# Optimization experiments

Measured on AMD Instinct MI355X. Metric: run time of the kernel, lower is better.

The kernel has to match this reference:

```python
import jax, jax.numpy as jnp
import numpy as np

HAND_PARAM_DIM = 32
MASK_THRESHOLD = 0.5
MAX_SAMPLES = 1024
INF_DIST = 1.0e6
EPS = 1e-8

B, S, HW, V = 4, 16, 65536, 778


def setup_inputs() -> dict:
    key = jax.random.key(0)
    ks = jax.random.split(key, 10)
    return {
        "hand_params": jax.random.normal(ks[0], (B, S, 2 * HAND_PARAM_DIM), jnp.float32),
        "gs_means": jax.random.normal(ks[1], (B, S, HW, 3), jnp.float32),
        "hand_gs_mask": jax.random.uniform(ks[2], (B, S, HW), jnp.float32),
        "hand_valid": jax.random.randint(ks[3], (B, S, 2), 0, 2).astype(jnp.int32),
        "v_template_l": jax.random.normal(ks[4], (V, 3), jnp.float32),
        "v_template_r": jax.random.normal(ks[5], (V, 3), jnp.float32),
        "shapedirs_l": jax.random.normal(ks[6], (V, 3, 10), jnp.float32) * 0.1,
        "shapedirs_r": jax.random.normal(ks[7], (V, 3, 10), jnp.float32) * 0.1,
        "posedirs_l": jax.random.normal(ks[8], (V, 3, 15), jnp.float32) * 0.1,
        "posedirs_r": jax.random.normal(ks[9], (V, 3, 15), jnp.float32) * 0.1,
    }


def quat_wxyz_to_rotvec(q):
    # q: [..., 4] (w, x, y, z) -> rotvec [..., 3]; faithful to the torch impl.
    q_norm = jnp.sqrt(jnp.sum(q * q, axis=-1, keepdims=True) + EPS)
    q = q / jnp.maximum(q_norm, EPS)
    w = q[..., 0:1]
    xyz = q[..., 1:4]
    sign = jnp.where(w < 0, -1.0, 1.0)
    w = w * sign
    xyz = xyz * sign
    sin_half = jnp.sqrt(jnp.sum(xyz * xyz, axis=-1, keepdims=True) + EPS)
    w_safe = jnp.clip(w, -1.0 + EPS, 1.0 - EPS)
    angle = 2.0 * jnp.arctan2(sin_half, w_safe)
    factor = jnp.where(sin_half < 1e-6, 2.0, angle / jnp.maximum(sin_half, EPS))
    return xyz * factor


def _rodrigues(pts, rotvec):
    # pts: [N, V, 3], rotvec: [N, 3]
    angle = jnp.sqrt(jnp.sum(rotvec * rotvec, axis=-1, keepdims=True) + EPS)  # [N,1]
    axis = rotvec / angle                                                      # [N,3]
    c = jnp.cos(angle)[:, None, :]   # [N,1,1]
    s = jnp.sin(angle)[:, None, :]
    k = axis[:, None, :]             # [N,1,3]
    kxv = jnp.cross(jnp.broadcast_to(k, pts.shape), pts)
    kdv = jnp.sum(k * pts, axis=-1, keepdims=True)
    return pts * c + kxv * s + k * kdv * (1.0 - c)


def _mano_points(p, v_template, shapedirs, posedirs):
    # p: [N, 32] -> points [N, V, 3] (linear MANO surrogate: template + blend dirs,
    # globally rotated by quaternion->rotvec and translated).
    transl = p[:, :3]
    q = p[:, 3:7]
    hand_pose = p[:, 7:22]
    betas = p[:, 22:32]
    rotvec = quat_wxyz_to_rotvec(q)
    pts = (v_template[None]
           + jnp.einsum('vck,nk->nvc', shapedirs, betas)
           + jnp.einsum('vck,nk->nvc', posedirs, hand_pose))
    return _rodrigues(pts, rotvec) + transl[:, None, :]


def reference(hand_params, gs_means, hand_gs_mask, hand_valid,
              v_template_l, v_template_r, shapedirs_l, shapedirs_r,
              posedirs_l, posedirs_r):
    b, s = hand_params.shape[:2]
    hw = gs_means.shape[2]
    bs = b * s
    params_flat = hand_params.reshape(bs, 2, HAND_PARAM_DIM)
    hv = hand_valid.reshape(bs, 2).astype(bool)

    left_pts = _mano_points(params_flat[:, 0], v_template_l, shapedirs_l, posedirs_l)
    right_pts = _mano_points(params_flat[:, 1], v_template_r, shapedirs_r, posedirs_r)
    left_pts = jnp.where(hv[:, 0:1, None], left_pts, INF_DIST)
    right_pts = jnp.where(hv[:, 1:2, None], right_pts, INF_DIST)
    mesh_pts = jnp.concatenate([left_pts, right_pts], axis=1)   # [BS, 2V, 3]

    k = min(MAX_SAMPLES, hw)
    mask_flat = hand_gs_mask.reshape(bs, hw)
    means_flat = gs_means.reshape(bs, hw, 3)
    top_vals, top_idx = jax.lax.top_k(mask_flat, k)             # [BS, K]
    sel_valid = (top_vals > MASK_THRESHOLD) & jnp.any(hv, axis=-1, keepdims=True)
    sampled = jnp.take_along_axis(means_flat, top_idx[..., None], axis=1)  # [BS, K, 3]

    # squared euclidean distances via gram trick: [BS, K, 2V]
    sa = jnp.sum(sampled * sampled, axis=-1)
    sb = jnp.sum(mesh_pts * mesh_pts, axis=-1)
    d2 = jnp.maximum(sa[:, :, None] + sb[:, None, :]
                     - 2.0 * jnp.einsum('nkc,npc->nkp', sampled, mesh_pts), 0.0)
    nn_d2 = jnp.min(d2, axis=-1)                                 # [BS, K]

    w = sel_valid.astype(nn_d2.dtype)
    num_samples = jnp.maximum(jnp.sum(w), 1.0)
    return jnp.sum(nn_d2 * w) / num_samples
```

## Files before the change

kernel.cpp:

```cpp
#include <hip/hip_runtime.h>
#include <math.h>

#define HAND_PARAM_DIM 32
#define INF_DIST 1000000.0f
#define EPS 1e-8f
#define NROW 64
#define HW_N 65536
#define NV 778
#define NMESH 1556
#define NMESH_PAD 1568
#define SLICE 98
#define NSLICE 16
#define K_SEL 1024u
#define HALF_BITS  0x3F000000u
#define GUESS_BITS 0x3F733333u
#define TOP_BITS   0x3F800000u
#define CHUNK_SLOT 512
#define CAND_MAX   8192
#define FIX_SCALE 4294967296.0

#define OFF_CAND 0u
#define OFF_CCNT 4194304u
#define OFF_CTR  4198400u
#define OFF_MESH 4198416u
#define OFF_SAMP 5804048u
#define OFF_MINP 6852624u

typedef unsigned long long u64;

__global__ void __launch_bounds__(256) combo_kernel(
    const float* __restrict__ mask, const int* __restrict__ hv,
    u64* __restrict__ cand, unsigned* __restrict__ ccnt,
    const float* __restrict__ hp,
    const float* __restrict__ vtl, const float* __restrict__ vtr,
    const float* __restrict__ sdl, const float* __restrict__ sdr,
    const float* __restrict__ pdl, const float* __restrict__ pdr,
    float4* __restrict__ meshP)
{
    int blk = blockIdx.x;
    int t = threadIdx.x;

    if (blk < 1024) {
        __shared__ u64 loc[CHUNK_SLOT];
        __shared__ unsigned nc, nbad;
        int row = blk >> 4, chunk = blk & 15;
        if (!(hv[row*2] | hv[row*2+1])) return;
        if (t == 0) { nc = 0u; nbad = 0u; }
        __syncthreads();
        const float4* m4 = (const float4*)(mask + (size_t)row * HW_N + chunk * 4096);
#pragma unroll
        for (int k = 0; k < 4; k++) {
            float4 v = m4[k*256 + t];
            unsigned e0 = (unsigned)(chunk*4096 + k*1024 + t*4);
            unsigned u;
            u = __float_as_uint(v.x);
            if (u >= GUESS_BITS) { unsigned p = atomicAdd(&nc,1u); if (p < CHUNK_SLOT) loc[p] = ((u64)u<<32)|(e0+0u); if (u >= TOP_BITS) nbad = 1u; }
            u = __float_as_uint(v.y);
            if (u >= GUESS_BITS) { unsigned p = atomicAdd(&nc,1u); if (p < CHUNK_SLOT) loc[p] = ((u64)u<<32)|(e0+1u); if (u >= TOP_BITS) nbad = 1u; }
            u = __float_as_uint(v.z);
            if (u >= GUESS_BITS) { unsigned p = atomicAdd(&nc,1u); if (p < CHUNK_SLOT) loc[p] = ((u64)u<<32)|(e0+2u); if (u >= TOP_BITS) nbad = 1u; }
            u = __float_as_uint(v.w);
            if (u >= GUESS_BITS) { unsigned p = atomicAdd(&nc,1u); if (p < CHUNK_SLOT) loc[p] = ((u64)u<<32)|(e0+3u); if (u >= TOP_BITS) nbad = 1u; }
        }
        __syncthreads();
        unsigned n = (nc < CHUNK_SLOT) ? nc : CHUNK_SLOT;
        if (t == 0) ccnt[row*16 + chunk] = nc | (nbad << 31);
        u64* dst = cand + ((size_t)(row*16 + chunk)) * CHUNK_SLOT;
        for (unsigned i = t; i < n; i += 256) dst[i] = loc[i];
        return;
    }

    int mb   = blk - 1024;
    int row  = mb >> 1;
    int hand = mb & 1;
    const float* p = hp + row * (2 * HAND_PARAM_DIM) + hand * HAND_PARAM_DIM;
    int valid = hv[row * 2 + hand];

    const float* vt = hand ? vtr : vtl;
    const float* sd = hand ? sdr : sdl;
    const float* pd = hand ? pdr : pdl;

    if (hand == 1 && t < (NMESH_PAD - NMESH))
        meshP[row * NMESH_PAD + NMESH + t] = make_float4(0.f, 0.f, 0.f, 3.4e38f);

    float tx = p[0], ty = p[1], tz = p[2];
    float q0 = p[3], q1 = p[4], q2 = p[5], q3 = p[6];
    float qn = sqrtf(q0*q0 + q1*q1 + q2*q2 + q3*q3 + EPS);
    float inv = 1.0f / fmaxf(qn, EPS);
    q0 *= inv; q1 *= inv; q2 *= inv; q3 *= inv;
    float sgn = (q0 < 0.0f) ? -1.0f : 1.0f;
    q0 *= sgn; q1 *= sgn; q2 *= sgn; q3 *= sgn;
    float sin_half = sqrtf(q1*q1 + q2*q2 + q3*q3 + EPS);
    float w_safe = fminf(fmaxf(q0, -1.0f + EPS), 1.0f - EPS);
    float ang2 = 2.0f * atan2f(sin_half, w_safe);
    float factor = (sin_half < 1e-6f) ? 2.0f : ang2 / fmaxf(sin_half, EPS);
    float rx = q1 * factor, ry = q2 * factor, rz = q3 * factor;
    float ang = sqrtf(rx*rx + ry*ry + rz*rz + EPS);
    float iang = 1.0f / ang;
    float ax = rx * iang, ay = ry * iang, az = rz * iang;
    float c = cosf(ang), s = sinf(ang), omc = 1.0f - c;

    float pose[15], betas[10];
#pragma unroll
    for (int k = 0; k < 15; k++) pose[k] = p[7 + k];
#pragma unroll
    for (int k = 0; k < 10; k++) betas[k] = p[22 + k];

    for (int v = t; v < NV; v += 256) {
        float px = vt[v*3+0], py = vt[v*3+1], pz = vt[v*3+2];
        const float* sdv = sd + v * 30;
#pragma unroll
        for (int k = 0; k < 10; k++) {
            px = fmaf(sdv[k],      betas[k], px);
            py = fmaf(sdv[10 + k], betas[k], py);
            pz = fmaf(sdv[20 + k], betas[k], pz);
        }
        const float* pdv = pd + v * 45;
#pragma unroll
        for (int k = 0; k < 15; k++) {
            px = fmaf(pdv[k],      pose[k], px);
            py = fmaf(pdv[15 + k], pose[k], py);
            pz = fmaf(pdv[30 + k], pose[k], pz);
        }
        float cx = ay * pz - az * py;
        float cy = az * px - ax * pz;
        float cz = ax * py - ay * px;
        float kdv = ax * px + ay * py + az * pz;
        float ox = px * c + cx * s + ax * kdv * omc + tx;
        float oy = py * c + cy * s + ay * kdv * omc + ty;
        float oz = pz * c + cz * s + az * kdv * omc + tz;
        if (!valid) { ox = INF_DIST; oy = INF_DIST; oz = INF_DIST; }
        float sb = fmaf(ox, ox, fmaf(oy, oy, oz * oz));
        meshP[row * NMESH_PAD + hand * NV + v] = make_float4(-2.0f*ox, -2.0f*oy, -2.0f*oz, sb);
    }
}

__global__ void __launch_bounds__(256) sel_fin_kernel(
    const float* __restrict__ mask, const float* __restrict__ means,
    const int* __restrict__ hv,
    const u64* __restrict__ cand, const unsigned* __restrict__ ccnt,
    float4* __restrict__ sampbuf, unsigned* __restrict__ ctr)
{
    __shared__ unsigned cval[CAND_MAX], cidx[CAND_MAX];
    __shared__ unsigned h[256], seg[256];
    __shared__ unsigned csub[16], cbase[16];
    __shared__ unsigned sbin, sRn, sbad, stot;
    __shared__ unsigned tlist[256];
    __shared__ unsigned tn, ns, scut;
    int row = blockIdx.x, t = threadIdx.x;

    if (row == 0 && t < 4) ctr[t] = 0u;
    for (unsigned i = t; i < K_SEL; i += 256)
        sampbuf[(size_t)row * K_SEL + i] = make_float4(0.f, 0.f, 0.f, -1.0f);
    if (!(hv[row*2] | hv[row*2+1])) return;

    if (t == 0) { sbad = 0u; tn = 0u; ns = 0u; }
    __syncthreads();
    if (t < 16) {
        unsigned w = ccnt[row*16 + t];
        unsigned n = w & 0x7FFFFFFFu;
        csub[t] = (n < CHUNK_SLOT) ? n : CHUNK_SLOT;
        if ((w >> 31) || n > CHUNK_SLOT) atomicOr(&sbad, 1u);
    }
    __syncthreads();
    if (t == 0) {
        unsigned run = 0;
#pragma unroll
        for (int c = 0; c < 16; c++) { cbase[c] = run; run += csub[c]; }
        stot = run;
    }
    __syncthreads();
    unsigned cnt = stot;
    bool ok = (sbad == 0u) && (cnt >= K_SEL) && (cnt <= CAND_MAX);
    const float* mrow = mask + (size_t)row * HW_N;
    unsigned M = ok ? cnt : (unsigned)HW_N;

    if (ok) {
#pragma unroll
        for (int c = 0; c < 16; c++) {
            unsigned n = csub[c], b = cbase[c];
            const u64* src = cand + ((size_t)(row*16 + c)) * CHUNK_SLOT;
            for (unsigned i = t; i < n; i += 256) {
                u64 e = src[i];
                cval[b + i] = (unsigned)(e >> 32); cidx[b + i] = (unsigned)e;
            }
        }
    }
    __syncthreads();

    unsigned T, R;
    if (ok) {
        unsigned pfx = 0u; R = K_SEL;
        for (int ph = 0; ph < 2; ph++) {
            int sh = 8 * (1 - ph);
            h[t] = 0u;
            __syncthreads();
            for (unsigned i = t; i < cnt; i += 256) {
                unsigned off = cval[i] - GUESS_BITS;
                if (ph == 0 || (off >> 8) == pfx) atomicAdd(&h[(off >> sh) & 0xFFu], 1u);
            }
            __syncthreads();
            seg[t] = h[t];
            __syncthreads();
            for (int off2 = 1; off2 < 256; off2 <<= 1) {
                unsigned v = (t + off2 < 256) ? seg[t + off2] : 0u;
                __syncthreads(); seg[t] += v; __syncthreads();
            }
            unsigned excl = (t < 255) ? seg[t + 1] : 0u;
            if (excl < R && R <= seg[t]) { sbin = (unsigned)t; sRn = R - excl; }
            __syncthreads();
            pfx = (ph == 0) ? sbin : ((pfx << 8) | sbin);
            R = sRn;
            __syncthreads();
        }
        T = GUESS_BITS + pfx;
    } else {
        unsigned pfx = 0u; R = K_SEL;
        for (int ph = 0; ph < 4; ph++) {
            int sh = 24 - 8 * ph;
            unsigned pm = (ph == 0) ? 0u : (0xFFFFFFFFu << (sh + 8));
            h[t] = 0u;
            __syncthreads();
            for (unsigned i = t; i < M; i += 256) {
                unsigned u = __float_as_uint(mrow[i]);
                if ((u & pm) == pfx) atomicAdd(&h[(u >> sh) & 0xFFu], 1u);
            }
            __syncthreads();
            seg[t] = h[t];
            __syncthreads();
            for (int off2 = 1; off2 < 256; off2 <<= 1) {
                unsigned v = (t + off2 < 256) ? seg[t + off2] : 0u;
                __syncthreads(); seg[t] += v; __syncthreads();
            }
            unsigned excl = (t < 255) ? seg[t + 1] : 0u;
            if (excl < R && R <= seg[t]) { sbin = (unsigned)t; sRn = R - excl; }
            __syncthreads();
            pfx |= sbin << sh;
            R = sRn;
            __syncthreads();
        }
        T = pfx;
    }

    for (unsigned i = t; i < M; i += 256) {
        unsigned u = ok ? cval[i] : __float_as_uint(mrow[i]);
        if (u == T) {
            unsigned p = atomicAdd(&tn, 1u);
            if (p < 256u) tlist[p] = ok ? cidx[i] : i;
        }
    }
    __syncthreads();
    if (t == 0) {
        unsigned n2 = (tn < 256u) ? tn : 256u;
        for (unsigned a = 1; a < n2; a++) {
            unsigned key = tlist[a]; int b = (int)a - 1;
            while (b >= 0 && tlist[b] > key) { tlist[b+1] = tlist[b]; b--; }
            tlist[b+1] = key;
        }
        unsigned r = R;
        if (r > n2) r = n2;
        if (r < 1u) r = 1u;
        scut = (n2 > 0u) ? tlist[r - 1] : 0u;
    }
    __syncthreads();
    unsigned cut = scut;
    for (unsigned i = t; i < M; i += 256) {
        unsigned u  = ok ? cval[i] : __float_as_uint(mrow[i]);
        unsigned id = ok ? cidx[i] : i;
        if (u > T || (u == T && id <= cut)) {
            unsigned p = atomicAdd(&ns, 1u);
            if (p < K_SEL) {
                const float* gm = means + ((size_t)row * HW_N + id) * 3;
                float sx = gm[0], sy = gm[1], sz = gm[2];
                float sa = fmaf(sx, sx, fmaf(sy, sy, sz * sz));
                float w  = (u > HALF_BITS) ? sa : -1.0f;
                sampbuf[(size_t)row * K_SEL + p] = make_float4(sx, sy, sz, w);
            }
        }
    }
}

__global__ void __launch_bounds__(128) dist_kernel(
    const float4* __restrict__ meshP, const float4* __restrict__ sampbuf,
    float* __restrict__ minpart)
{
    __shared__ float4 mq[SLICE];
    int blk = blockIdx.x;
    int r = blk >> 4, sl = blk & 15;
    int t = threadIdx.x;

    if (t < SLICE) mq[t] = meshP[r * NMESH_PAD + sl * SLICE + t];

    const float4* sb = sampbuf + (size_t)r * K_SEL;
    float sx[8], sy[8], sz[8], mn[8];
#pragma unroll
    for (int k = 0; k < 8; k++) {
        float4 s = sb[t + 128*k];
        sx[k] = s.x; sy[k] = s.y; sz[k] = s.z;
        mn[k] = 3.4e38f;
    }
    __syncthreads();

#pragma unroll 2
    for (int i = 0; i < SLICE; i++) {
        float4 a = mq[i];
#pragma unroll
        for (int k = 0; k < 8; k++)
            mn[k] = fminf(mn[k], fmaf(sx[k], a.x, fmaf(sy[k], a.y, fmaf(sz[k], a.z, a.w))));
    }

    float* mp = minpart + ((size_t)r * NSLICE + sl) * K_SEL;
#pragma unroll
    for (int k = 0; k < 8; k++) mp[t + 128*k] = mn[k];
}

__global__ void __launch_bounds__(256) reduce_kernel(
    const float* __restrict__ minpart, const float4* __restrict__ sampbuf,
    unsigned* __restrict__ ctr, float* __restrict__ out)
{
    __shared__ long long rs[256];
    __shared__ unsigned rc[256];
    int row = blockIdx.x;
    int t = threadIdx.x;

    long long acc = 0; unsigned c = 0;
#pragma unroll
    for (int k = 0; k < 4; k++) {
        int j = k * 256 + t;
        const float* mp = minpart + (size_t)row * NSLICE * K_SEL + j;
        float m = mp[0];
#pragma unroll
        for (int s = 1; s < NSLICE; s++) m = fminf(m, mp[s * (int)K_SEL]);
        float4 sp = sampbuf[(size_t)row * K_SEL + j];
        if (sp.w >= 0.0f) {
            float d2 = fmaxf(m + sp.w, 0.0f);
            acc += (long long)((double)d2 * FIX_SCALE);
            c += 1u;
        }
    }
    rs[t] = acc; rc[t] = c;
    __syncthreads();
    for (int off = 128; off > 0; off >>= 1) {
        if (t < off) { rs[t] += rs[t+off]; rc[t] += rc[t+off]; }
        __syncthreads();
    }
    if (t == 0) {
        atomicAdd((u64*)ctr, (u64)rs[0]);
        atomicAdd(&ctr[2], rc[0]);
        __threadfence();
        unsigned tk = atomicAdd(&ctr[3], 1u);
        if (tk == (unsigned)(NROW - 1)) {
            u64 sbits = atomicAdd((u64*)ctr, 0ull);
            unsigned cc = atomicAdd(&ctr[2], 0u);
            double sum = (double)(long long)sbits / FIX_SCALE;
            out[0] = (float)(sum / (double)(cc ? cc : 1u));
        }
    }
}

extern "C" void kernel_launch(void* const* d_in, const int* in_sizes, int n_in,
                              void* d_out, int out_size, void* d_ws, size_t ws_size,
                              hipStream_t stream) {
    const float* hp    = (const float*)d_in[0];
    const float* means = (const float*)d_in[1];
    const float* mask  = (const float*)d_in[2];
    const int*   hv    = (const int*)  d_in[3];
    const float* vtl   = (const float*)d_in[4];
    const float* vtr   = (const float*)d_in[5];
    const float* sdl   = (const float*)d_in[6];
    const float* sdr   = (const float*)d_in[7];
    const float* pdl   = (const float*)d_in[8];
    const float* pdr   = (const float*)d_in[9];
    float* out = (float*)d_out;

    char* ws = (char*)d_ws;
    u64*      cand    = (u64*)(ws + OFF_CAND);
    unsigned* ccnt    = (unsigned*)(ws + OFF_CCNT);
    unsigned* ctr     = (unsigned*)(ws + OFF_CTR);
    float4*   meshP   = (float4*)(ws + OFF_MESH);
    float4*   sampbuf = (float4*)(ws + OFF_SAMP);
    float*    minpart = (float*)(ws + OFF_MINP);

    combo_kernel<<<1024 + 128, 256, 0, stream>>>(mask, hv, cand, ccnt,
                                                 hp, vtl, vtr, sdl, sdr, pdl, pdr, meshP);
    sel_fin_kernel<<<NROW, 256, 0, stream>>>(mask, means, hv, cand, ccnt, sampbuf, ctr);
    dist_kernel<<<NROW * NSLICE, 128, 0, stream>>>(meshP, sampbuf, minpart);
    reduce_kernel<<<NROW, 256, 0, stream>>>(minpart, sampbuf, ctr, out);
}
```

Measured before the change: 57.01 us.

## Fuse candidate scan, mesh build and top-k select into one row kernel

Merges the chunked mask-candidate kernel, the mesh-construction blocks and the selection kernel into a single 1024-thread block per row. Candidates stay in per-wave shared-memory lists, so the global candidate buffer round trip and one launch go away. Output order is made deterministic through per-wave counts and prefix offsets. The cost is that the 4 MB mask scan now runs on only 64 blocks instead of 1024, so per-row serial work and lower parallelism may offset the saved launch and traffic.

```diff
diff --git a/kernel.cpp b/kernel.cpp
--- a/kernel.cpp
+++ b/kernel.cpp
@@ -14,113 +14,86 @@
 #define K_SEL 1024u
 #define HALF_BITS  0x3F000000u
 #define GUESS_BITS 0x3F733333u
-#define TOP_BITS   0x3F800000u
-#define CHUNK_SLOT 512
-#define CAND_MAX   8192
+#define W_CAP 512
+#define NWAVE 16
 #define FIX_SCALE 4294967296.0
 
-#define OFF_CAND 0u
-#define OFF_CCNT 4194304u
-#define OFF_CTR  4198400u
-#define OFF_MESH 4198416u
-#define OFF_SAMP 5804048u
-#define OFF_MINP 6852624u
+#define OFF_MESH 0u
+#define OFF_SAMP 1605632u
+#define OFF_MINP 2654208u
+#define OFF_CTR  6848512u
 
 typedef unsigned long long u64;
 
-__global__ void __launch_bounds__(256) combo_kernel(
-    const float* __restrict__ mask, const int* __restrict__ hv,
-    u64* __restrict__ cand, unsigned* __restrict__ ccnt,
-    const float* __restrict__ hp,
+__global__ void __launch_bounds__(1024) prep_kernel(
+    const float* __restrict__ mask, const float* __restrict__ means,
+    const int* __restrict__ hv, const float* __restrict__ hp,
     const float* __restrict__ vtl, const float* __restrict__ vtr,
     const float* __restrict__ sdl, const float* __restrict__ sdr,
     const float* __restrict__ pdl, const float* __restrict__ pdr,
-    float4* __restrict__ meshP)
+    float4* __restrict__ meshP, float4* __restrict__ sampbuf,
+    unsigned* __restrict__ ctr)
 {
-    int blk = blockIdx.x;
-    int t = threadIdx.x;
-
-    if (blk < 1024) {
-        __shared__ u64 loc[CHUNK_SLOT];
-        __shared__ unsigned nc, nbad;
-        int row = blk >> 4, chunk = blk & 15;
-        if (!(hv[row*2] | hv[row*2+1])) return;
-        if (t == 0) { nc = 0u; nbad = 0u; }
-        __syncthreads();
-        const float4* m4 = (const float4*)(mask + (size_t)row * HW_N + chunk * 4096);
-#pragma unroll
-        for (int k = 0; k < 4; k++) {
-            float4 v = m4[k*256 + t];
-            unsigned e0 = (unsigned)(chunk*4096 + k*1024 + t*4);
-            unsigned u;
-            u = __float_as_uint(v.x);
-            if (u >= GUESS_BITS) { unsigned p = atomicAdd(&nc,1u); if (p < CHUNK_SLOT) loc[p] = ((u64)u<<32)|(e0+0u); if (u >= TOP_BITS) nbad = 1u; }
-            u = __float_as_uint(v.y);
-            if (u >= GUESS_BITS) { unsigned p = atomicAdd(&nc,1u); if (p < CHUNK_SLOT) loc[p] = ((u64)u<<32)|(e0+1u); if (u >= TOP_BITS) nbad = 1u; }
-            u = __float_as_uint(v.z);
-            if (u >= GUESS_BITS) { unsigned p = atomicAdd(&nc,1u); if (p < CHUNK_SLOT) loc[p] = ((u64)u<<32)|(e0+2u); if (u >= TOP_BITS) nbad = 1u; }
-            u = __float_as_uint(v.w);
-            if (u >= GUESS_BITS) { unsigned p = atomicAdd(&nc,1u); if (p < CHUNK_SLOT) loc[p] = ((u64)u<<32)|(e0+3u); if (u >= TOP_BITS) nbad = 1u; }
-        }
-        __syncthreads();
-        unsigned n = (nc < CHUNK_SLOT) ? nc : CHUNK_SLOT;
-        if (t == 0) ccnt[row*16 + chunk] = nc | (nbad << 31);
-        u64* dst = cand + ((size_t)(row*16 + chunk)) * CHUNK_SLOT;
-        for (unsigned i = t; i < n; i += 256) dst[i] = loc[i];
-        return;
-    }
-
-    int mb   = blk - 1024;
-    int row  = mb >> 1;
-    int hand = mb & 1;
-    const float* p = hp + row * (2 * HAND_PARAM_DIM) + hand * HAND_PARAM_DIM;
-    int valid = hv[row * 2 + hand];
-
-    const float* vt = hand ? vtr : vtl;
-    const float* sd = hand ? sdr : sdl;
-    const float* pd = hand ? pdr : pdl;
-
-    if (hand == 1 && t < (NMESH_PAD - NMESH))
-        meshP[row * NMESH_PAD + NMESH + t] = make_float4(0.f, 0.f, 0.f, 3.4e38f);
-
-    float tx = p[0], ty = p[1], tz = p[2];
-    float q0 = p[3], q1 = p[4], q2 = p[5], q3 = p[6];
-    float qn = sqrtf(q0*q0 + q1*q1 + q2*q2 + q3*q3 + EPS);
-    float inv = 1.0f / fmaxf(qn, EPS);
-    q0 *= inv; q1 *= inv; q2 *= inv; q3 *= inv;
-    float sgn = (q0 < 0.0f) ? -1.0f : 1.0f;
-    q0 *= sgn; q1 *= sgn; q2 *= sgn; q3 *= sgn;
-    float sin_half = sqrtf(q1*q1 + q2*q2 + q3*q3 + EPS);
-    float w_safe = fminf(fmaxf(q0, -1.0f + EPS), 1.0f - EPS);
-    float ang2 = 2.0f * atan2f(sin_half, w_safe);
-    float factor = (sin_half < 1e-6f) ? 2.0f : ang2 / fmaxf(sin_half, EPS);
-    float rx = q1 * factor, ry = q2 * factor, rz = q3 * factor;
-    float ang = sqrtf(rx*rx + ry*ry + rz*rz + EPS);
-    float iang = 1.0f / ang;
-    float ax = rx * iang, ay = ry * iang, az = rz * iang;
-    float c = cosf(ang), s = sinf(ang), omc = 1.0f - c;
-
-    float pose[15], betas[10];
-#pragma unroll
-    for (int k = 0; k < 15; k++) pose[k] = p[7 + k];
-#pragma unroll
-    for (int k = 0; k < 10; k++) betas[k] = p[22 + k];
-
-    for (int v = t; v < NV; v += 256) {
+    __shared__ u64 cl[NWAVE * W_CAP];
+    __shared__ unsigned wcnt[NWAVE], wsel[NWAVE], wpos[NWAVE];
+    __shared__ unsigned h[256], seg[256];
+    __shared__ unsigned tlist[256];
+    __shared__ unsigned sbin, sRn, sbad, stot, tn, scut;
+
+    int row = blockIdx.x, t = threadIdx.x;
+    int wave = t >> 6;
+
+    if (row == 0 && t < 4) ctr[t] = 0u;
+    sampbuf[(size_t)row * K_SEL + t] = make_float4(0.f, 0.f, 0.f, -1.0f);
+    int hv0 = hv[row*2], hv1 = hv[row*2+1];
+    if (!(hv0 | hv1)) return;
+
+    for (int slot = t; slot < NMESH_PAD; slot += 1024) {
+        if (slot >= NMESH) {
+            meshP[row * NMESH_PAD + slot] = make_float4(0.f, 0.f, 0.f, 3.4e38f);
+            continue;
+        }
+        int hand = (slot >= NV) ? 1 : 0;
+        int v = slot - hand * NV;
+        const float* p = hp + row * (2 * HAND_PARAM_DIM) + hand * HAND_PARAM_DIM;
+        int valid = hand ? hv1 : hv0;
+        const float* vt = hand ? vtr : vtl;
+        const float* sd = hand ? sdr : sdl;
+        const float* pd = hand ? pdr : pdl;
+
+        float tx = p[0], ty = p[1], tz = p[2];
+        float q0 = p[3], q1 = p[4], q2 = p[5], q3 = p[6];
+        float qn = sqrtf(q0*q0 + q1*q1 + q2*q2 + q3*q3 + EPS);
+        float inv = 1.0f / fmaxf(qn, EPS);
+        q0 *= inv; q1 *= inv; q2 *= inv; q3 *= inv;
+        float sgn = (q0 < 0.0f) ? -1.0f : 1.0f;
+        q0 *= sgn; q1 *= sgn; q2 *= sgn; q3 *= sgn;
+        float sin_half = sqrtf(q1*q1 + q2*q2 + q3*q3 + EPS);
+        float w_safe = fminf(fmaxf(q0, -1.0f + EPS), 1.0f - EPS);
+        float ang2 = 2.0f * atan2f(sin_half, w_safe);
+        float factor = (sin_half < 1e-6f) ? 2.0f : ang2 / fmaxf(sin_half, EPS);
+        float rx = q1 * factor, ry = q2 * factor, rz = q3 * factor;
+        float ang = sqrtf(rx*rx + ry*ry + rz*rz + EPS);
+        float iang = 1.0f / ang;
+        float ax = rx * iang, ay = ry * iang, az = rz * iang;
+        float c = cosf(ang), s = sinf(ang), omc = 1.0f - c;
+
         float px = vt[v*3+0], py = vt[v*3+1], pz = vt[v*3+2];
         const float* sdv = sd + v * 30;
 #pragma unroll
         for (int k = 0; k < 10; k++) {
-            px = fmaf(sdv[k],      betas[k], px);
-            py = fmaf(sdv[10 + k], betas[k], py);
-            pz = fmaf(sdv[20 + k], betas[k], pz);
+            float b = p[22 + k];
+            px = fmaf(sdv[k],      b, px);
+            py = fmaf(sdv[10 + k], b, py);
+            pz = fmaf(sdv[20 + k], b, pz);
         }
         const float* pdv = pd + v * 45;
 #pragma unroll
         for (int k = 0; k < 15; k++) {
-            px = fmaf(pdv[k],      pose[k], px);
-            py = fmaf(pdv[15 + k], pose[k], py);
-            pz = fmaf(pdv[30 + k], pose[k], pz);
+            float o = p[7 + k];
+            px = fmaf(pdv[k],      o, px);
+            py = fmaf(pdv[15 + k], o, py);
+            pz = fmaf(pdv[30 + k], o, pz);
         }
         float cx = ay * pz - az * py;
         float cy = az * px - ax * pz;
@@ -131,83 +104,68 @@
         float oz = pz * c + cz * s + az * kdv * omc + tz;
         if (!valid) { ox = INF_DIST; oy = INF_DIST; oz = INF_DIST; }
         float sb = fmaf(ox, ox, fmaf(oy, oy, oz * oz));
-        meshP[row * NMESH_PAD + hand * NV + v] = make_float4(-2.0f*ox, -2.0f*oy, -2.0f*oz, sb);
-    }
-}
-
-__global__ void __launch_bounds__(256) sel_fin_kernel(
-    const float* __restrict__ mask, const float* __restrict__ means,
-    const int* __restrict__ hv,
-    const u64* __restrict__ cand, const unsigned* __restrict__ ccnt,
-    float4* __restrict__ sampbuf, unsigned* __restrict__ ctr)
-{
-    __shared__ unsigned cval[CAND_MAX], cidx[CAND_MAX];
-    __shared__ unsigned h[256], seg[256];
-    __shared__ unsigned csub[16], cbase[16];
-    __shared__ unsigned sbin, sRn, sbad, stot;
-    __shared__ unsigned tlist[256];
-    __shared__ unsigned tn, ns, scut;
-    int row = blockIdx.x, t = threadIdx.x;
-
-    if (row == 0 && t < 4) ctr[t] = 0u;
-    for (unsigned i = t; i < K_SEL; i += 256)
-        sampbuf[(size_t)row * K_SEL + i] = make_float4(0.f, 0.f, 0.f, -1.0f);
-    if (!(hv[row*2] | hv[row*2+1])) return;
-
-    if (t == 0) { sbad = 0u; tn = 0u; ns = 0u; }
-    __syncthreads();
-    if (t < 16) {
-        unsigned w = ccnt[row*16 + t];
-        unsigned n = w & 0x7FFFFFFFu;
-        csub[t] = (n < CHUNK_SLOT) ? n : CHUNK_SLOT;
-        if ((w >> 31) || n > CHUNK_SLOT) atomicOr(&sbad, 1u);
+        meshP[row * NMESH_PAD + slot] = make_float4(-2.0f*ox, -2.0f*oy, -2.0f*oz, sb);
+    }
+
+    if (t < NWAVE) wcnt[t] = 0u;
+    if (t == 0) { sbad = 0u; tn = 0u; }
+    __syncthreads();
+    const float* mrow = mask + (size_t)row * HW_N;
+    const float4* m4 = (const float4*)mrow;
+#pragma unroll 4
+    for (int k = 0; k < 16; k++) {
+        float4 v = m4[k * 1024 + t];
+        unsigned e0 = (unsigned)((k * 1024 + t) * 4);
+        unsigned u;
+#define PROC(comp, off_) { u = __float_as_uint(comp); \
+        if (u - GUESS_BITS < 0x10000u) { \
+            unsigned p_ = atomicAdd(&wcnt[wave], 1u); \
+            if (p_ < W_CAP) cl[(wave << 9) + p_] = ((u64)u << 32) | (e0 + off_); \
+        } else if (u >= GUESS_BITS + 0x10000u && u < 0x80000000u) sbad = 1u; }
+        PROC(v.x, 0u) PROC(v.y, 1u) PROC(v.z, 2u) PROC(v.w, 3u)
+#undef PROC
     }
     __syncthreads();
     if (t == 0) {
         unsigned run = 0;
 #pragma unroll
-        for (int c = 0; c < 16; c++) { cbase[c] = run; run += csub[c]; }
+        for (int c2 = 0; c2 < NWAVE; c2++) {
+            unsigned n = wcnt[c2];
+            if (n > W_CAP) { sbad = 1u; n = W_CAP; wcnt[c2] = n; }
+            run += n;
+        }
         stot = run;
     }
     __syncthreads();
-    unsigned cnt = stot;
-    bool ok = (sbad == 0u) && (cnt >= K_SEL) && (cnt <= CAND_MAX);
-    const float* mrow = mask + (size_t)row * HW_N;
-    unsigned M = ok ? cnt : (unsigned)HW_N;
-
-    if (ok) {
-#pragma unroll
-        for (int c = 0; c < 16; c++) {
-            unsigned n = csub[c], b = cbase[c];
-            const u64* src = cand + ((size_t)(row*16 + c)) * CHUNK_SLOT;
-            for (unsigned i = t; i < n; i += 256) {
-                u64 e = src[i];
-                cval[b + i] = (unsigned)(e >> 32); cidx[b + i] = (unsigned)e;
-            }
-        }
-    }
-    __syncthreads();
+    bool ok = (sbad == 0u) && (stot >= K_SEL);
 
     unsigned T, R;
     if (ok) {
         unsigned pfx = 0u; R = K_SEL;
         for (int ph = 0; ph < 2; ph++) {
-            int sh = 8 * (1 - ph);
-            h[t] = 0u;
-            __syncthreads();
-            for (unsigned i = t; i < cnt; i += 256) {
-                unsigned off = cval[i] - GUESS_BITS;
-                if (ph == 0 || (off >> 8) == pfx) atomicAdd(&h[(off >> sh) & 0xFFu], 1u);
-            }
-            __syncthreads();
-            seg[t] = h[t];
-            __syncthreads();
-            for (int off2 = 1; off2 < 256; off2 <<= 1) {
-                unsigned v = (t + off2 < 256) ? seg[t + off2] : 0u;
-                __syncthreads(); seg[t] += v; __syncthreads();
-            }
-            unsigned excl = (t < 255) ? seg[t + 1] : 0u;
-            if (excl < R && R <= seg[t]) { sbin = (unsigned)t; sRn = R - excl; }
+            if (t < 256) h[t] = 0u;
+            __syncthreads();
+            for (int i = t; i < NWAVE * W_CAP; i += 1024) {
+                if ((unsigned)(i & (W_CAP - 1)) < wcnt[i >> 9]) {
+                    unsigned off = (unsigned)(cl[i] >> 32) - GUESS_BITS;
+                    if (ph == 0) atomicAdd(&h[off >> 8], 1u);
+                    else if ((off >> 8) == pfx) atomicAdd(&h[off & 0xFFu], 1u);
+                }
+            }
+            __syncthreads();
+            if (t < 256) seg[t] = h[t];
+            __syncthreads();
+            for (int o = 1; o < 256; o <<= 1) {
+                unsigned v = 0u;
+                if (t < 256 && t + o < 256) v = seg[t + o];
+                __syncthreads();
+                if (t < 256) seg[t] += v;
+                __syncthreads();
+            }
+            if (t < 256) {
+                unsigned excl = (t < 255) ? seg[t + 1] : 0u;
+                if (excl < R && R <= seg[t]) { sbin = (unsigned)t; sRn = R - excl; }
+            }
             __syncthreads();
             pfx = (ph == 0) ? sbin : ((pfx << 8) | sbin);
             R = sRn;
@@ -219,21 +177,26 @@
         for (int ph = 0; ph < 4; ph++) {
             int sh = 24 - 8 * ph;
             unsigned pm = (ph == 0) ? 0u : (0xFFFFFFFFu << (sh + 8));
-            h[t] = 0u;
-            __syncthreads();
-            for (unsigned i = t; i < M; i += 256) {
+            if (t < 256) h[t] = 0u;
+            __syncthreads();
+            for (int i = t; i < HW_N; i += 1024) {
                 unsigned u = __float_as_uint(mrow[i]);
                 if ((u & pm) == pfx) atomicAdd(&h[(u >> sh) & 0xFFu], 1u);
             }
             __syncthreads();
-            seg[t] = h[t];
-            __syncthreads();
-            for (int off2 = 1; off2 < 256; off2 <<= 1) {
-                unsigned v = (t + off2 < 256) ? seg[t + off2] : 0u;
-                __syncthreads(); seg[t] += v; __syncthreads();
-            }
-            unsigned excl = (t < 255) ? seg[t + 1] : 0u;
-            if (excl < R && R <= seg[t]) { sbin = (unsigned)t; sRn = R - excl; }
+            if (t < 256) seg[t] = h[t];
+            __syncthreads();
+            for (int o = 1; o < 256; o <<= 1) {
+                unsigned v = 0u;
+                if (t < 256 && t + o < 256) v = seg[t + o];
+                __syncthreads();
+                if (t < 256) seg[t] += v;
+                __syncthreads();
+            }
+            if (t < 256) {
+                unsigned excl = (t < 255) ? seg[t + 1] : 0u;
+                if (excl < R && R <= seg[t]) { sbin = (unsigned)t; sRn = R - excl; }
+            }
             __syncthreads();
             pfx |= sbin << sh;
             R = sRn;
@@ -242,11 +205,22 @@
         T = pfx;
     }
 
-    for (unsigned i = t; i < M; i += 256) {
-        unsigned u = ok ? cval[i] : __float_as_uint(mrow[i]);
-        if (u == T) {
-            unsigned p = atomicAdd(&tn, 1u);
-            if (p < 256u) tlist[p] = ok ? cidx[i] : i;
+    if (ok) {
+        for (int i = t; i < NWAVE * W_CAP; i += 1024) {
+            if ((unsigned)(i & (W_CAP - 1)) < wcnt[i >> 9]) {
+                u64 e = cl[i];
+                if ((unsigned)(e >> 32) == T) {
+                    unsigned p_ = atomicAdd(&tn, 1u);
+                    if (p_ < 256u) tlist[p_] = (unsigned)e;
+                }
+            }
+        }
+    } else {
+        for (int i = t; i < HW_N; i += 1024) {
+            if (__float_as_uint(mrow[i]) == T) {
+                unsigned p_ = atomicAdd(&tn, 1u);
+                if (p_ < 256u) tlist[p_] = (unsigned)i;
+            }
         }
     }
     __syncthreads();
@@ -262,19 +236,60 @@
         if (r < 1u) r = 1u;
         scut = (n2 > 0u) ? tlist[r - 1] : 0u;
     }
+    if (t < NWAVE) wsel[t] = 0u;
     __syncthreads();
     unsigned cut = scut;
-    for (unsigned i = t; i < M; i += 256) {
-        unsigned u  = ok ? cval[i] : __float_as_uint(mrow[i]);
-        unsigned id = ok ? cidx[i] : i;
-        if (u > T || (u == T && id <= cut)) {
-            unsigned p = atomicAdd(&ns, 1u);
-            if (p < K_SEL) {
-                const float* gm = means + ((size_t)row * HW_N + id) * 3;
-                float sx = gm[0], sy = gm[1], sz = gm[2];
-                float sa = fmaf(sx, sx, fmaf(sy, sy, sz * sz));
-                float w  = (u > HALF_BITS) ? sa : -1.0f;
-                sampbuf[(size_t)row * K_SEL + p] = make_float4(sx, sy, sz, w);
+
+    if (ok) {
+        for (int i = t; i < NWAVE * W_CAP; i += 1024) {
+            if ((unsigned)(i & (W_CAP - 1)) < wcnt[i >> 9]) {
+                u64 e = cl[i];
+                unsigned u = (unsigned)(e >> 32), id = (unsigned)e;
+                if (u > T || (u == T && id <= cut)) atomicAdd(&wsel[wave], 1u);
+            }
+        }
+    } else {
+        for (int i = t; i < HW_N; i += 1024) {
+            unsigned u = __float_as_uint(mrow[i]);
+            if (u > T || (u == T && (unsigned)i <= cut)) atomicAdd(&wsel[wave], 1u);
+        }
+    }
+    __syncthreads();
+    if (t == 0) {
+        unsigned run = 0;
+#pragma unroll
+        for (int c2 = 0; c2 < NWAVE; c2++) { wpos[c2] = run; run += wsel[c2]; }
+    }
+    __syncthreads();
+    if (ok) {
+        for (int i = t; i < NWAVE * W_CAP; i += 1024) {
+            if ((unsigned)(i & (W_CAP - 1)) < wcnt[i >> 9]) {
+                u64 e = cl[i];
+                unsigned u = (unsigned)(e >> 32), id = (unsigned)e;
+                if (u > T || (u == T && id <= cut)) {
+                    unsigned p_ = atomicAdd(&wpos[wave], 1u);
+                    if (p_ < K_SEL) {
+                        const float* gm = means + ((size_t)row * HW_N + id) * 3;
+                        float sx = gm[0], sy = gm[1], sz = gm[2];
+                        float sa = fmaf(sx, sx, fmaf(sy, sy, sz * sz));
+                        float w  = (u > HALF_BITS) ? sa : -1.0f;
+                        sampbuf[(size_t)row * K_SEL + p_] = make_float4(sx, sy, sz, w);
+                    }
+                }
+            }
+        }
+    } else {
+        for (int i = t; i < HW_N; i += 1024) {
+            unsigned u = __float_as_uint(mrow[i]);
+            if (u > T || (u == T && (unsigned)i <= cut)) {
+                unsigned p_ = atomicAdd(&wpos[wave], 1u);
+                if (p_ < K_SEL) {
+                    const float* gm = means + ((size_t)row * HW_N + i) * 3;
+                    float sx = gm[0], sy = gm[1], sz = gm[2];
+                    float sa = fmaf(sx, sx, fmaf(sy, sy, sz * sz));
+                    float w  = (u > HALF_BITS) ? sa : -1.0f;
+                    sampbuf[(size_t)row * K_SEL + p_] = make_float4(sx, sy, sz, w);
+                }
             }
         }
     }
@@ -374,16 +389,14 @@
     float* out = (float*)d_out;
 
     char* ws = (char*)d_ws;
-    u64*      cand    = (u64*)(ws + OFF_CAND);
-    unsigned* ccnt    = (unsigned*)(ws + OFF_CCNT);
-    unsigned* ctr     = (unsigned*)(ws + OFF_CTR);
     float4*   meshP   = (float4*)(ws + OFF_MESH);
     float4*   sampbuf = (float4*)(ws + OFF_SAMP);
     float*    minpart = (float*)(ws + OFF_MINP);
-
-    combo_kernel<<<1024 + 128, 256, 0, stream>>>(mask, hv, cand, ccnt,
-                                                 hp, vtl, vtr, sdl, sdr, pdl, pdr, meshP);
-    sel_fin_kernel<<<NROW, 256, 0, stream>>>(mask, means, hv, cand, ccnt, sampbuf, ctr);
+    unsigned* ctr     = (unsigned*)(ws + OFF_CTR);
+
+    prep_kernel<<<NROW, 1024, 0, stream>>>(mask, means, hv, hp,
+                                           vtl, vtr, sdl, sdr, pdl, pdr,
+                                           meshP, sampbuf, ctr);
     dist_kernel<<<NROW * NSLICE, 128, 0, stream>>>(meshP, sampbuf, minpart);
     reduce_kernel<<<NROW, 256, 0, stream>>>(minpart, sampbuf, ctr, out);
 }
```

Measured after the change: 165.3 us. 2.9x slower.

## Fuse distance and reduction kernels via per-row last-block ticket, halve slices

Applied to the files above, without the earlier changes.

Merges the separate reduce kernel into the distance kernel. The last slice block of each row, found with an atomic ticket counter that sel_fin_kernel resets, does that row's min-over-slices and sum reduction. The mesh is split into 8 slices of 196 points instead of 16 of 98, so there are half as many blocks, each doing more work, and fewer partial minima to reduce. This removes one kernel launch and its dependency gap, but adds fences and atomics, and leaves 512 blocks to fill the GPU.

```diff
diff --git a/kernel.cpp b/kernel.cpp
--- a/kernel.cpp
+++ b/kernel.cpp
@@ -9,8 +9,8 @@
 #define NV 778
 #define NMESH 1556
 #define NMESH_PAD 1568
-#define SLICE 98
-#define NSLICE 16
+#define SLICE 196
+#define NSLICE 8
 #define K_SEL 1024u
 #define HALF_BITS  0x3F000000u
 #define GUESS_BITS 0x3F733333u
@@ -22,9 +22,10 @@
 #define OFF_CAND 0u
 #define OFF_CCNT 4194304u
 #define OFF_CTR  4198400u
-#define OFF_MESH 4198416u
-#define OFF_SAMP 5804048u
-#define OFF_MINP 6852624u
+#define OFF_TICK 4198416u
+#define OFF_MESH 4198672u
+#define OFF_SAMP 5804304u
+#define OFF_MINP 6852880u
 
 typedef unsigned long long u64;
 
@@ -51,16 +52,15 @@
 #pragma unroll
         for (int k = 0; k < 4; k++) {
             float4 v = m4[k*256 + t];
-            unsigned e0 = (unsigned)(chunk*4096 + k*1024 + t*4);
+            unsigned e0 = (unsigned)(chunk*4096 + (k*256 + t)*4);
             unsigned u;
-            u = __float_as_uint(v.x);
-            if (u >= GUESS_BITS) { unsigned p = atomicAdd(&nc,1u); if (p < CHUNK_SLOT) loc[p] = ((u64)u<<32)|(e0+0u); if (u >= TOP_BITS) nbad = 1u; }
-            u = __float_as_uint(v.y);
-            if (u >= GUESS_BITS) { unsigned p = atomicAdd(&nc,1u); if (p < CHUNK_SLOT) loc[p] = ((u64)u<<32)|(e0+1u); if (u >= TOP_BITS) nbad = 1u; }
-            u = __float_as_uint(v.z);
-            if (u >= GUESS_BITS) { unsigned p = atomicAdd(&nc,1u); if (p < CHUNK_SLOT) loc[p] = ((u64)u<<32)|(e0+2u); if (u >= TOP_BITS) nbad = 1u; }
-            u = __float_as_uint(v.w);
-            if (u >= GUESS_BITS) { unsigned p = atomicAdd(&nc,1u); if (p < CHUNK_SLOT) loc[p] = ((u64)u<<32)|(e0+3u); if (u >= TOP_BITS) nbad = 1u; }
+#define PROC(comp, off_) { u = __float_as_uint(comp); \
+            if (u >= GUESS_BITS) { \
+                unsigned p_ = atomicAdd(&nc, 1u); \
+                if (p_ < CHUNK_SLOT) loc[p_] = ((u64)u << 32) | (e0 + off_); \
+                if (u >= TOP_BITS) nbad = 1u; } }
+            PROC(v.x, 0u) PROC(v.y, 1u) PROC(v.z, 2u) PROC(v.w, 3u)
+#undef PROC
         }
         __syncthreads();
         unsigned n = (nc < CHUNK_SLOT) ? nc : CHUNK_SLOT;
@@ -139,7 +139,8 @@
     const float* __restrict__ mask, const float* __restrict__ means,
     const int* __restrict__ hv,
     const u64* __restrict__ cand, const unsigned* __restrict__ ccnt,
-    float4* __restrict__ sampbuf, unsigned* __restrict__ ctr)
+    float4* __restrict__ sampbuf, unsigned* __restrict__ ctr,
+    unsigned* __restrict__ rowtick)
 {
     __shared__ unsigned cval[CAND_MAX], cidx[CAND_MAX];
     __shared__ unsigned h[256], seg[256];
@@ -150,6 +151,7 @@
     int row = blockIdx.x, t = threadIdx.x;
 
     if (row == 0 && t < 4) ctr[t] = 0u;
+    if (t == 0) rowtick[row] = 0u;
     for (unsigned i = t; i < K_SEL; i += 256)
         sampbuf[(size_t)row * K_SEL + i] = make_float4(0.f, 0.f, 0.f, -1.0f);
     if (!(hv[row*2] | hv[row*2+1])) return;
@@ -280,18 +282,22 @@
     }
 }
 
-__global__ void __launch_bounds__(128) dist_kernel(
+__global__ void __launch_bounds__(128) dist_red_kernel(
     const float4* __restrict__ meshP, const float4* __restrict__ sampbuf,
-    float* __restrict__ minpart)
+    float* __restrict__ minpart, unsigned* __restrict__ rowtick,
+    unsigned* __restrict__ ctr, float* __restrict__ out)
 {
     __shared__ float4 mq[SLICE];
+    __shared__ long long rs[128];
+    __shared__ unsigned rc[128];
+    __shared__ unsigned stick;
     int blk = blockIdx.x;
-    int r = blk >> 4, sl = blk & 15;
+    int row = blk >> 3, sl = blk & 7;
     int t = threadIdx.x;
 
-    if (t < SLICE) mq[t] = meshP[r * NMESH_PAD + sl * SLICE + t];
-
-    const float4* sb = sampbuf + (size_t)r * K_SEL;
+    for (int i = t; i < SLICE; i += 128) mq[i] = meshP[row * NMESH_PAD + sl * SLICE + i];
+
+    const float4* sb = sampbuf + (size_t)row * K_SEL;
     float sx[8], sy[8], sz[8], mn[8];
 #pragma unroll
     for (int k = 0; k < 8; k++) {
@@ -309,29 +315,25 @@
             mn[k] = fminf(mn[k], fmaf(sx[k], a.x, fmaf(sy[k], a.y, fmaf(sz[k], a.z, a.w))));
     }
 
-    float* mp = minpart + ((size_t)r * NSLICE + sl) * K_SEL;
+    float* mp = minpart + ((size_t)row * NSLICE + sl) * K_SEL;
 #pragma unroll
     for (int k = 0; k < 8; k++) mp[t + 128*k] = mn[k];
-}
-
-__global__ void __launch_bounds__(256) reduce_kernel(
-    const float* __restrict__ minpart, const float4* __restrict__ sampbuf,
-    unsigned* __restrict__ ctr, float* __restrict__ out)
-{
-    __shared__ long long rs[256];
-    __shared__ unsigned rc[256];
-    int row = blockIdx.x;
-    int t = threadIdx.x;
+
+    __threadfence();
+    if (t == 0) stick = atomicAdd(&rowtick[row], 1u);
+    __syncthreads();
+    if (stick != (unsigned)(NSLICE - 1)) return;
+    __threadfence();
 
     long long acc = 0; unsigned c = 0;
 #pragma unroll
-    for (int k = 0; k < 4; k++) {
-        int j = k * 256 + t;
-        const float* mp = minpart + (size_t)row * NSLICE * K_SEL + j;
-        float m = mp[0];
-#pragma unroll
-        for (int s = 1; s < NSLICE; s++) m = fminf(m, mp[s * (int)K_SEL]);
-        float4 sp = sampbuf[(size_t)row * K_SEL + j];
+    for (int k = 0; k < 8; k++) {
+        int j = k * 128 + t;
+        const float* q = minpart + (size_t)row * NSLICE * K_SEL + j;
+        float m = q[0];
+#pragma unroll
+        for (int s = 1; s < NSLICE; s++) m = fminf(m, q[s * (int)K_SEL]);
+        float4 sp = sb[j];
         if (sp.w >= 0.0f) {
             float d2 = fmaxf(m + sp.w, 0.0f);
             acc += (long long)((double)d2 * FIX_SCALE);
@@ -340,7 +342,7 @@
     }
     rs[t] = acc; rc[t] = c;
     __syncthreads();
-    for (int off = 128; off > 0; off >>= 1) {
+    for (int off = 64; off > 0; off >>= 1) {
         if (t < off) { rs[t] += rs[t+off]; rc[t] += rc[t+off]; }
         __syncthreads();
     }
@@ -348,8 +350,8 @@
         atomicAdd((u64*)ctr, (u64)rs[0]);
         atomicAdd(&ctr[2], rc[0]);
         __threadfence();
-        unsigned tk = atomicAdd(&ctr[3], 1u);
-        if (tk == (unsigned)(NROW - 1)) {
+        unsigned dk = atomicAdd(&ctr[3], 1u);
+        if (dk == (unsigned)(NROW - 1)) {
             u64 sbits = atomicAdd((u64*)ctr, 0ull);
             unsigned cc = atomicAdd(&ctr[2], 0u);
             double sum = (double)(long long)sbits / FIX_SCALE;
@@ -377,13 +379,15 @@
     u64*      cand    = (u64*)(ws + OFF_CAND);
     unsigned* ccnt    = (unsigned*)(ws + OFF_CCNT);
     unsigned* ctr     = (unsigned*)(ws + OFF_CTR);
+    unsigned* rowtick = (unsigned*)(ws + OFF_TICK);
     float4*   meshP   = (float4*)(ws + OFF_MESH);
     float4*   sampbuf = (float4*)(ws + OFF_SAMP);
     float*    minpart = (float*)(ws + OFF_MINP);
 
     combo_kernel<<<1024 + 128, 256, 0, stream>>>(mask, hv, cand, ccnt,
                                                  hp, vtl, vtr, sdl, sdr, pdl, pdr, meshP);
-    sel_fin_kernel<<<NROW, 256, 0, stream>>>(mask, means, hv, cand, ccnt, sampbuf, ctr);
-    dist_kernel<<<NROW * NSLICE, 128, 0, stream>>>(meshP, sampbuf, minpart);
-    reduce_kernel<<<NROW, 256, 0, stream>>>(minpart, sampbuf, ctr, out);
+    sel_fin_kernel<<<NROW, 256, 0, stream>>>(mask, means, hv, cand, ccnt,
+                                             sampbuf, ctr, rowtick);
+    dist_red_kernel<<<NROW * NSLICE, 128, 0, stream>>>(meshP, sampbuf, minpart,
+                                                       rowtick, ctr, out);
 }
```

New measurement: 93.60 us. +64.2%, slower.
